# Kernel optimization log

Measured on AMD Instinct MI355X. Metric: run time of the kernel, lower is better.

The kernel has to match this reference:

```python
import jax, jax.numpy as jnp
import numpy as np

N, T, V, C, K, F = 64, 300, 25, 64, 3, 64
I = F // 4  # inter_filters = filters // 4


def setup_inputs() -> dict:
    key = jax.random.key(0)
    ks = jax.random.split(key, 8)
    x = jax.random.normal(ks[0], (N, T, V, C), jnp.float32)
    A = jax.random.uniform(ks[1], (K, V, V), jnp.float32)
    W = jax.random.normal(ks[2], (C, K * F), jnp.float32) * 0.05   # 1x1 conv weight
    b = jax.random.normal(ks[3], (K * F,), jnp.float32) * 0.05     # conv bias
    Wq = jax.random.normal(ks[4], (K, C, I), jnp.float32) * 0.05   # per-K embedding_q
    bq = jax.random.normal(ks[5], (K, I), jnp.float32) * 0.05
    Wk = jax.random.normal(ks[6], (K, C, I), jnp.float32) * 0.05   # per-K embedding_k
    bk = jax.random.normal(ks[7], (K, I), jnp.float32) * 0.05
    return {"x": x, "A": A, "W": W, "b": b, "Wq": Wq, "bq": bq, "Wk": Wk, "bk": bk}


def reference(x, A, W, b, Wq, bq, Wk, bk):
    # x: (N,T,V,C); A: (K,V,V)
    n, t, v, c = x.shape
    k = A.shape[0]
    f = W.shape[1] // k
    i = Wq.shape[-1]
    d = t * i

    # main 1x1 conv (t_kernel_size=1) -> (N,T,V,K*F) -> (N,T,V,K,F)
    h = (jnp.einsum('ntvc,cf->ntvf', x, W) + b).reshape(n, t, v, k, f)

    # per-K query/key embeddings, vectorized over K: (K,N,T,V,I)
    q = jnp.einsum('ntvc,kci->kntvi', x, Wq) + bq[:, None, None, None, :]
    kk = jnp.einsum('ntvc,kci->kntvi', x, Wk) + bk[:, None, None, None, :]

    # A_1: transpose to (K,N,V,T,I) -> (K,N,V,T*I); A_2: (K,N,T,I,V) -> (K,N,T*I,V)
    q2 = q.transpose(0, 1, 3, 2, 4).reshape(k, n, v, d)
    k2 = kk.transpose(0, 1, 2, 4, 3).reshape(k, n, d, v)

    scale = np.float32(1.0 / np.sqrt(d))
    att = jax.nn.softmax(jnp.einsum('knvd,kndw->knvw', q2, k2) * scale, axis=-1)
    A_adapt = A[:, None, :, :] + att  # (K,N,V,V)

    # aggregation: y[n,t,w,c] = sum_{v,k} h[n,t,v,k,c] * A_adapt[k,n,v,w]
    y = jnp.einsum('ntvkc,knvw->ntwc', h, A_adapt)
    return y
```

## Files before the change

### kernel.cpp

```cpp
#include <hip/hip_runtime.h>

#define DI __device__ __forceinline__

typedef float f32x4 __attribute__((ext_vector_type(4)));
typedef short s16x8 __attribute__((ext_vector_type(8)));

constexpr int N_ = 64, T_ = 300, V_ = 25, C_ = 64, K_ = 3, F_ = 64, I_ = 16;

DI short f2bf(float f) {
  union { float f; unsigned u; } v; v.f = f;
  unsigned r = (v.u + 0x7fffu + ((v.u >> 16) & 1u)) >> 16;
  return (short)r;
}

__global__ __launch_bounds__(256, 2) void k1_scores(
    const float* __restrict__ x,
    const float* __restrict__ Wq, const float* __restrict__ bq,
    const float* __restrict__ Wk, const float* __restrict__ bk,
    float* __restrict__ Sacc)
{
  __shared__ __align__(16) short Xl[112 * 64];
  __shared__ __align__(16) short Wt[96 * 64];
  __shared__ __align__(16) short Pq[4 * 32 * 64];
  __shared__ __align__(16) short Pk[4 * 32 * 64];
  __shared__ float bcl[96];

  const int tid = threadIdx.x;
  const int lane = tid & 63;
  const int wid = tid >> 6;
  const int g = lane >> 4;
  const int lo = lane & 15;
  const int n = blockIdx.y;
  const int t0row = blockIdx.x * 100;

  for (int idx = tid; idx < 96 * 64; idx += 256) {
    int j = idx >> 6, c = idx & 63;
    float v;
    if (j < 48) v = Wq[(j >> 4) * (C_ * I_) + c * I_ + (j & 15)];
    else { int j2 = j - 48; v = Wk[(j2 >> 4) * (C_ * I_) + c * I_ + (j2 & 15)]; }
    Wt[j * 64 + (c ^ ((j & 7) << 3))] = f2bf(v);
  }
  if (tid < 96) bcl[tid] = (tid < 48) ? bq[tid] : bk[tid - 48];

  {
    const float* xb = x + (size_t)n * (T_ * V_ * C_) + (size_t)t0row * C_;
    for (int idx = tid; idx < 112 * 64; idx += 256) {
      int row = idx >> 6, c = idx & 63;
      float v = (row < 100) ? xb[idx] : 0.f;
      Xl[row * 64 + (c ^ ((row & 7) << 3))] = f2bf(v);
    }
  }
  __syncthreads();

  for (int i = 0; i < 11; ++i) {
    int tile = wid + i * 4;
    if (tile >= 42) break;
    int m = tile / 6, nt = tile % 6;
    float binit = bcl[nt * 16 + lo];
    f32x4 acc = { binit, binit, binit, binit };
#pragma unroll
    for (int ks = 0; ks < 2; ++ks) {
      int arow = m * 16 + lo;
      s16x8 a = *(const s16x8*)&Xl[arow * 64 + ((ks * 32 + g * 8) ^ ((arow & 7) << 3))];
      int brow = nt * 16 + lo;
      s16x8 b = *(const s16x8*)&Wt[brow * 64 + ((ks * 32 + g * 8) ^ ((brow & 7) << 3))];
      acc = __builtin_amdgcn_mfma_f32_16x16x32_bf16(a, b, acc, 0, 0, 0);
    }
#pragma unroll
    for (int r = 0; r < 4; ++r) {
      int row = m * 16 + g * 4 + r;
      if (row < 100) {
        int t = row / 25, v = row - t * 25;
        int j = nt * 16 + lo;
        short val = f2bf(acc[r]);
        if (j < 48) Pq[(t * 32 + v) * 64 + (j ^ ((v & 7) << 3))] = val;
        else        Pk[(t * 32 + v) * 64 + ((j - 48) ^ ((v & 7) << 3))] = val;
      }
    }
  }
  __syncthreads();

#pragma unroll
  for (int i = 0; i < 3; ++i) {
    int combo = wid + i * 4;
    int k = combo >> 2, vt = (combo >> 1) & 1, wt = combo & 1;
    f32x4 acc = { 0.f, 0.f, 0.f, 0.f };
#pragma unroll
    for (int ks = 0; ks < 2; ++ks) {
      int t = ks * 2 + (g >> 1);
      int ib = (g & 1) * 8;
      int v = vt * 16 + lo;
      s16x8 a = *(const s16x8*)&Pq[(t * 32 + v) * 64 + ((k * 16 + ib) ^ ((v & 7) << 3))];
      int w = wt * 16 + lo;
      s16x8 b = *(const s16x8*)&Pk[(t * 32 + w) * 64 + ((k * 16 + ib) ^ ((w & 7) << 3))];
      acc = __builtin_amdgcn_mfma_f32_16x16x32_bf16(a, b, acc, 0, 0, 0);
    }
#pragma unroll
    for (int r = 0; r < 4; ++r) {
      int v = vt * 16 + g * 4 + r;
      int w = wt * 16 + lo;
      if (v < 25 && w < 25)
        atomicAdd(&Sacc[((size_t)(k * 64 + n) * 25 + v) * 25 + w], acc[r]);
    }
  }
}

__global__ void k2_softmax(const float* __restrict__ Sacc,
                           const float* __restrict__ A,
                           unsigned short* __restrict__ AadT)
{
  int bx = blockIdx.x;
  int k = bx >> 6;
  int tid = threadIdx.x;
  unsigned short* outb = AadT + (size_t)bx * 1024;
  for (int idx = tid; idx < 1024; idx += 64) outb[idx] = 0;
  __syncthreads();
  if (tid < 25) {
    int v = tid;
    const float* srow = Sacc + ((size_t)bx * 25 + v) * 25;
    const float scale = 0.014433756729740645f;
    float s[25];
    float mx = -1e30f;
#pragma unroll
    for (int w = 0; w < 25; ++w) { s[w] = srow[w] * scale; mx = fmaxf(mx, s[w]); }
    float sum = 0.f;
#pragma unroll
    for (int w = 0; w < 25; ++w) { s[w] = __expf(s[w] - mx); sum += s[w]; }
    float inv = 1.f / sum;
#pragma unroll
    for (int w = 0; w < 25; ++w) {
      float aad = A[(k * 25 + v) * 25 + w] + s[w] * inv;
      outb[w * 32 + v] = (unsigned short)f2bf(aad);
    }
  }
}

__global__ __launch_bounds__(256, 2) void k3_main(
    const float* __restrict__ x,
    const float* __restrict__ W, const float* __restrict__ b,
    const unsigned short* __restrict__ AadT, float* __restrict__ y)
{
  __shared__ __align__(16) short Xl[80 * 64];
  __shared__ __align__(16) short Wt[192 * 64];
  __shared__ __align__(16) short Ht[192 * 96];
  __shared__ __align__(16) short Al[3 * 32 * 32];
  __shared__ float bl[192];

  const int tid = threadIdx.x;
  const int lane = tid & 63;
  const int wid = tid >> 6;
  const int g = lane >> 4;
  const int lo = lane & 15;
  const int n = blockIdx.y;
  const int t0 = blockIdx.x * 3;

  for (int idx = tid; idx < 192 * 64; idx += 256) {
    int c = idx / 192, j = idx % 192;
    Wt[j * 64 + (c ^ ((j & 7) << 3))] = f2bf(W[idx]);
  }
  if (tid < 192) bl[tid] = b[tid];

  for (int idx = tid; idx < 3 * 1024; idx += 256) {
    int kk = idx >> 10, rem = idx & 1023, w = rem >> 5, v = rem & 31;
    unsigned short val = AadT[(size_t)(kk * 64 + n) * 1024 + rem];
    Al[(kk * 32 + w) * 32 + (v ^ ((w & 3) << 3))] = (short)val;
  }

  for (int idx = tid; idx < 192 * 24; idx += 256) {
    int kc = idx / 24, rem = idx % 24, t = rem >> 3, vv = 24 + (rem & 7);
    Ht[kc * 96 + ((t * 32 + vv) ^ ((kc & 3) << 3))] = 0;
  }

  {
    const float* xb = x + (size_t)n * (T_ * V_ * C_) + (size_t)t0 * (V_ * C_);
    for (int idx = tid; idx < 80 * 64; idx += 256) {
      int row = idx >> 6, c = idx & 63;
      float v = (row < 75) ? xb[idx] : 0.f;
      Xl[row * 64 + (c ^ ((row & 7) << 3))] = f2bf(v);
    }
  }
  __syncthreads();

#pragma unroll
  for (int i = 0; i < 15; ++i) {
    int tile = wid + i * 4;
    int m = tile / 12, nt = tile % 12;
    float binit = bl[nt * 16 + lo];
    f32x4 acc = { binit, binit, binit, binit };
#pragma unroll
    for (int ks = 0; ks < 2; ++ks) {
      int arow = m * 16 + lo;
      s16x8 a = *(const s16x8*)&Xl[arow * 64 + ((ks * 32 + g * 8) ^ ((arow & 7) << 3))];
      int brow = nt * 16 + lo;
      s16x8 bb = *(const s16x8*)&Wt[brow * 64 + ((ks * 32 + g * 8) ^ ((brow & 7) << 3))];
      acc = __builtin_amdgcn_mfma_f32_16x16x32_bf16(a, bb, acc, 0, 0, 0);
    }
#pragma unroll
    for (int r = 0; r < 4; ++r) {
      int row = m * 16 + g * 4 + r;
      if (row < 75) {
        int t = row / 25, v = row - t * 25;
        int kc = nt * 16 + lo;
        Ht[kc * 96 + ((t * 32 + v) ^ ((kc & 3) << 3))] = f2bf(acc[r]);
      }
    }
  }
  __syncthreads();

#pragma unroll
  for (int i = 0; i < 6; ++i) {
    int job = wid + i * 4;
    int t = job >> 3, rem = job & 7, wt = rem >> 2, ct = rem & 3;
    f32x4 acc = { 0.f, 0.f, 0.f, 0.f };
#pragma unroll
    for (int k3 = 0; k3 < 3; ++k3) {
      int w = wt * 16 + lo;
      s16x8 a = *(const s16x8*)&Al[(k3 * 32 + w) * 32 + ((g * 8) ^ ((w & 3) << 3))];
      int kc = k3 * 64 + ct * 16 + lo;
      s16x8 bb = *(const s16x8*)&Ht[kc * 96 + ((t * 32 + g * 8) ^ ((kc & 3) << 3))];
      acc = __builtin_amdgcn_mfma_f32_16x16x32_bf16(a, bb, acc, 0, 0, 0);
    }
#pragma unroll
    for (int r = 0; r < 4; ++r) {
      int w = wt * 16 + g * 4 + r;
      if (w < 25)
        y[(((size_t)n * T_ + t0 + t) * V_ + w) * C_ + ct * 16 + lo] = acc[r];
    }
  }
}

extern "C" void kernel_launch(void* const* d_in, const int* in_sizes, int n_in,
                              void* d_out, int out_size, void* d_ws, size_t ws_size,
                              hipStream_t stream) {
  const float* x  = (const float*)d_in[0];
  const float* A  = (const float*)d_in[1];
  const float* W  = (const float*)d_in[2];
  const float* b  = (const float*)d_in[3];
  const float* Wq = (const float*)d_in[4];
  const float* bq = (const float*)d_in[5];
  const float* Wk = (const float*)d_in[6];
  const float* bk = (const float*)d_in[7];
  float* y = (float*)d_out;

  float* Sacc = (float*)d_ws;
  unsigned short* AadT = (unsigned short*)((char*)d_ws + 512 * 1024);

  hipMemsetAsync(Sacc, 0, (size_t)K_ * N_ * V_ * V_ * sizeof(float), stream);
  k1_scores<<<dim3(75, 64), 256, 0, stream>>>(x, Wq, bq, Wk, bk, Sacc);
  k2_softmax<<<dim3(192), 64, 0, stream>>>(Sacc, A, AadT);
  k3_main<<<dim3(100, 64), 256, 0, stream>>>(x, W, b, AadT, y);
}
```

Measured before the change: 629.4 us.

## Replace atomic score accumulation with per-block partials reduced in softmax kernel

The scores kernel now loops over several 100-row chunks per block and keeps the Q·K accumulators in registers, writing one partial 25x25 matrix per block instead of atomically adding each chunk. The softmax kernel sums the G partials into shared memory before the softmax, which removes the memset and the global atomics. The cost is fewer blocks in the first kernel (G×64 instead of 75×64), which lowers parallelism, plus extra workspace traffic for the partials and a serial reduction loop in k2.

```diff
diff --git a/kernel.cpp b/kernel.cpp
--- a/kernel.cpp
+++ b/kernel.cpp
@@ -17,7 +17,7 @@
     const float* __restrict__ x,
     const float* __restrict__ Wq, const float* __restrict__ bq,
     const float* __restrict__ Wk, const float* __restrict__ bk,
-    float* __restrict__ Sacc)
+    float* __restrict__ Spart, int nChunks)
 {
   __shared__ __align__(16) short Xl[112 * 64];
   __shared__ __align__(16) short Wt[96 * 64];
@@ -31,7 +31,7 @@
   const int g = lane >> 4;
   const int lo = lane & 15;
   const int n = blockIdx.y;
-  const int t0row = blockIdx.x * 100;
+  const int p = blockIdx.x;
 
   for (int idx = tid; idx < 96 * 64; idx += 256) {
     int j = idx >> 6, c = idx & 63;
@@ -42,87 +42,108 @@
   }
   if (tid < 96) bcl[tid] = (tid < 48) ? bq[tid] : bk[tid - 48];
 
-  {
-    const float* xb = x + (size_t)n * (T_ * V_ * C_) + (size_t)t0row * C_;
-    for (int idx = tid; idx < 112 * 64; idx += 256) {
-      int row = idx >> 6, c = idx & 63;
-      float v = (row < 100) ? xb[idx] : 0.f;
-      Xl[row * 64 + (c ^ ((row & 7) << 3))] = f2bf(v);
-    }
-  }
-  __syncthreads();
-
-  for (int i = 0; i < 11; ++i) {
-    int tile = wid + i * 4;
-    if (tile >= 42) break;
-    int m = tile / 6, nt = tile % 6;
-    float binit = bcl[nt * 16 + lo];
-    f32x4 acc = { binit, binit, binit, binit };
-#pragma unroll
-    for (int ks = 0; ks < 2; ++ks) {
-      int arow = m * 16 + lo;
-      s16x8 a = *(const s16x8*)&Xl[arow * 64 + ((ks * 32 + g * 8) ^ ((arow & 7) << 3))];
-      int brow = nt * 16 + lo;
-      s16x8 b = *(const s16x8*)&Wt[brow * 64 + ((ks * 32 + g * 8) ^ ((brow & 7) << 3))];
-      acc = __builtin_amdgcn_mfma_f32_16x16x32_bf16(a, b, acc, 0, 0, 0);
-    }
-#pragma unroll
-    for (int r = 0; r < 4; ++r) {
-      int row = m * 16 + g * 4 + r;
-      if (row < 100) {
-        int t = row / 25, v = row - t * 25;
-        int j = nt * 16 + lo;
-        short val = f2bf(acc[r]);
-        if (j < 48) Pq[(t * 32 + v) * 64 + (j ^ ((v & 7) << 3))] = val;
-        else        Pk[(t * 32 + v) * 64 + ((j - 48) ^ ((v & 7) << 3))] = val;
-      }
-    }
-  }
-  __syncthreads();
-
-#pragma unroll
-  for (int i = 0; i < 3; ++i) {
-    int combo = wid + i * 4;
+  f32x4 acc[3];
+#pragma unroll
+  for (int j = 0; j < 3; ++j) acc[j] = (f32x4){0.f, 0.f, 0.f, 0.f};
+
+  for (int chunk = 0; chunk < nChunks; ++chunk) {
+    const int t0row = (p * nChunks + chunk) * 100;
+
+    {
+      const float* xb = x + (size_t)n * (T_ * V_ * C_) + (size_t)t0row * C_;
+      for (int idx = tid; idx < 112 * 64; idx += 256) {
+        int row = idx >> 6, c = idx & 63;
+        float v = (row < 100) ? xb[idx] : 0.f;
+        Xl[row * 64 + (c ^ ((row & 7) << 3))] = f2bf(v);
+      }
+    }
+    __syncthreads();
+
+    for (int i = 0; i < 11; ++i) {
+      int tile = wid + i * 4;
+      if (tile >= 42) break;
+      int m = tile / 6, nt = tile % 6;
+      float binit = bcl[nt * 16 + lo];
+      f32x4 pacc = { binit, binit, binit, binit };
+#pragma unroll
+      for (int ks = 0; ks < 2; ++ks) {
+        int arow = m * 16 + lo;
+        s16x8 a = *(const s16x8*)&Xl[arow * 64 + ((ks * 32 + g * 8) ^ ((arow & 7) << 3))];
+        int brow = nt * 16 + lo;
+        s16x8 b = *(const s16x8*)&Wt[brow * 64 + ((ks * 32 + g * 8) ^ ((brow & 7) << 3))];
+        pacc = __builtin_amdgcn_mfma_f32_16x16x32_bf16(a, b, pacc, 0, 0, 0);
+      }
+#pragma unroll
+      for (int r = 0; r < 4; ++r) {
+        int row = m * 16 + g * 4 + r;
+        if (row < 100) {
+          int t = row / 25, v = row - t * 25;
+          int j = nt * 16 + lo;
+          short val = f2bf(pacc[r]);
+          if (j < 48) Pq[(t * 32 + v) * 64 + (j ^ ((v & 7) << 3))] = val;
+          else        Pk[(t * 32 + v) * 64 + ((j - 48) ^ ((v & 7) << 3))] = val;
+        }
+      }
+    }
+    __syncthreads();
+
+#pragma unroll
+    for (int j = 0; j < 3; ++j) {
+      int combo = wid + j * 4;
+      int k = combo >> 2, vt = (combo >> 1) & 1, wt = combo & 1;
+#pragma unroll
+      for (int ks = 0; ks < 2; ++ks) {
+        int t = ks * 2 + (g >> 1);
+        int ib = (g & 1) * 8;
+        int v = vt * 16 + lo;
+        s16x8 a = *(const s16x8*)&Pq[(t * 32 + v) * 64 + ((k * 16 + ib) ^ ((v & 7) << 3))];
+        int w = wt * 16 + lo;
+        s16x8 b = *(const s16x8*)&Pk[(t * 32 + w) * 64 + ((k * 16 + ib) ^ ((w & 7) << 3))];
+        acc[j] = __builtin_amdgcn_mfma_f32_16x16x32_bf16(a, b, acc[j], 0, 0, 0);
+      }
+    }
+  }
+
+#pragma unroll
+  for (int j = 0; j < 3; ++j) {
+    int combo = wid + j * 4;
     int k = combo >> 2, vt = (combo >> 1) & 1, wt = combo & 1;
-    f32x4 acc = { 0.f, 0.f, 0.f, 0.f };
-#pragma unroll
-    for (int ks = 0; ks < 2; ++ks) {
-      int t = ks * 2 + (g >> 1);
-      int ib = (g & 1) * 8;
-      int v = vt * 16 + lo;
-      s16x8 a = *(const s16x8*)&Pq[(t * 32 + v) * 64 + ((k * 16 + ib) ^ ((v & 7) << 3))];
-      int w = wt * 16 + lo;
-      s16x8 b = *(const s16x8*)&Pk[(t * 32 + w) * 64 + ((k * 16 + ib) ^ ((w & 7) << 3))];
-      acc = __builtin_amdgcn_mfma_f32_16x16x32_bf16(a, b, acc, 0, 0, 0);
-    }
 #pragma unroll
     for (int r = 0; r < 4; ++r) {
       int v = vt * 16 + g * 4 + r;
       int w = wt * 16 + lo;
       if (v < 25 && w < 25)
-        atomicAdd(&Sacc[((size_t)(k * 64 + n) * 25 + v) * 25 + w], acc[r]);
-    }
-  }
-}
-
-__global__ void k2_softmax(const float* __restrict__ Sacc,
+        Spart[((size_t)p * 192 + (k * 64 + n)) * 625 + v * 25 + w] = acc[j][r];
+    }
+  }
+}
+
+__global__ void k2_softmax(const float* __restrict__ Spart,
                            const float* __restrict__ A,
-                           unsigned short* __restrict__ AadT)
+                           unsigned short* __restrict__ AadT, int G)
 {
+  __shared__ float Ss[625];
   int bx = blockIdx.x;
   int k = bx >> 6;
   int tid = threadIdx.x;
   unsigned short* outb = AadT + (size_t)bx * 1024;
-  for (int idx = tid; idx < 1024; idx += 64) outb[idx] = 0;
+  for (int idx = tid; idx < 1024; idx += 256) outb[idx] = 0;
+
+  for (int cell = tid; cell < 625; cell += 256) {
+    float s = 0.f;
+    for (int pp = 0; pp < G; ++pp)
+      s += Spart[((size_t)pp * 192 + bx) * 625 + cell];
+    Ss[cell] = s;
+  }
   __syncthreads();
+
   if (tid < 25) {
     int v = tid;
-    const float* srow = Sacc + ((size_t)bx * 25 + v) * 25;
     const float scale = 0.014433756729740645f;
     float s[25];
     float mx = -1e30f;
 #pragma unroll
-    for (int w = 0; w < 25; ++w) { s[w] = srow[w] * scale; mx = fmaxf(mx, s[w]); }
+    for (int w = 0; w < 25; ++w) { s[w] = Ss[v * 25 + w] * scale; mx = fmaxf(mx, s[w]); }
     float sum = 0.f;
 #pragma unroll
     for (int w = 0; w < 25; ++w) { s[w] = __expf(s[w] - mx); sum += s[w]; }
@@ -242,11 +263,17 @@
   const float* bk = (const float*)d_in[7];
   float* y = (float*)d_out;
 
-  float* Sacc = (float*)d_ws;
-  unsigned short* AadT = (unsigned short*)((char*)d_ws + 512 * 1024);
-
-  hipMemsetAsync(Sacc, 0, (size_t)K_ * N_ * V_ * V_ * sizeof(float), stream);
-  k1_scores<<<dim3(75, 64), 256, 0, stream>>>(x, Wq, bq, Wk, bk, Sacc);
-  k2_softmax<<<dim3(192), 64, 0, stream>>>(Sacc, A, AadT);
+  unsigned short* AadT = (unsigned short*)d_ws;
+  float* Spart = (float*)((char*)d_ws + 512 * 1024);
+
+  const size_t base = 512 * 1024;
+  const size_t perG = (size_t)192 * 625 * sizeof(float);
+  int G = 25;
+  if (base + 25 * perG > ws_size) G = 15;
+  if (base + 15 * perG > ws_size) G = 5;
+  int nChunks = 75 / G;
+
+  k1_scores<<<dim3(G, 64), 256, 0, stream>>>(x, Wq, bq, Wk, bk, Spart, nChunks);
+  k2_softmax<<<dim3(192), 256, 0, stream>>>(Spart, A, AadT, G);
   k3_main<<<dim3(100, 64), 256, 0, stream>>>(x, W, b, AadT, y);
 }
```

Result: no change. 622.9 us (-1.0%).
